# Kernel optimization log

Measured on AMD Instinct MI355X. Metric: run time of the kernel, lower is better.

## Reference

```python
import jax, jax.numpy as jnp
import numpy as np
import math

B, T, C = 4, 2048, 1024
H = 16  # parallelAttentionPathways
D = C // H  # head dim = 64


def setup_inputs() -> dict:
    key = jax.random.key(0)
    k1, k2, k3 = jax.random.split(key, 3)
    x = jax.random.normal(k1, (B, T, C), dtype=jnp.float32)
    w_qkv = jax.random.normal(k2, (3 * C, C), dtype=jnp.float32) * (1.0 / math.sqrt(C))
    w_out = jax.random.normal(k3, (C, C), dtype=jnp.float32) * (1.0 / math.sqrt(C))
    return {"x": x, "w_qkv": w_qkv, "w_out": w_out}


def reference(x, w_qkv, w_out):
    b, t, c = x.shape
    # qkv projection: torch Linear y = x @ W^T (no bias)
    qkv = jnp.einsum('btc,fc->btf', x, w_qkv)  # [B,T,3C]
    q, k, v = jnp.split(qkv, 3, axis=-1)
    # [B,H,T,D]
    q = q.reshape(b, t, H, D).transpose(0, 2, 1, 3)
    k = k.reshape(b, t, H, D).transpose(0, 2, 1, 3)
    v = v.reshape(b, t, H, D).transpose(0, 2, 1, 3)
    scale = 1.0 / math.sqrt(D)
    att = jnp.einsum('bhqd,bhkd->bhqk', q, k) * scale  # [B,H,T,T]
    causal = jnp.tril(jnp.ones((t, t), dtype=bool))
    att = jnp.where(causal[None, None], att, -jnp.inf)
    att = jax.nn.softmax(att, axis=-1)
    # dropoutRate=0.0 -> dropout is identity (eval-mode determinism)
    y = jnp.einsum('bhqk,bhkd->bhqd', att, v)  # [B,H,T,D]
    y = y.transpose(0, 2, 1, 3).reshape(b, t, c)
    return jnp.einsum('btc,fc->btf', y, w_out)
```

## Files before the change

kernel.cpp:

```cpp
#include <hip/hip_runtime.h>
#include <hip/hip_bf16.h>
#include <stdint.h>


using bf16 = __hip_bfloat16;
typedef __attribute__((ext_vector_type(8))) __bf16 bf16x8;
typedef __attribute__((ext_vector_type(8))) unsigned short u16x8;
typedef __attribute__((ext_vector_type(4))) unsigned short u16x4;
typedef __attribute__((ext_vector_type(4))) float f32x4;
typedef unsigned short ushort_t;

#define MFMA16(a, b, c) __builtin_amdgcn_mfma_f32_16x16x32_bf16((a), (b), (c), 0, 0, 0)

__device__ __forceinline__ bf16x8 ld_frag(const ushort_t* p) {
  const u16x8 u = *(const u16x8*)p;
  return __builtin_bit_cast(bf16x8, u);
}

__device__ __forceinline__ ushort_t f2bf(float f) {
  return __builtin_bit_cast(ushort_t, __float2bfloat16(f));
}

__device__ __forceinline__ void gl2lds16(const void* g, void* lds) {
  __builtin_amdgcn_global_load_lds((const __attribute__((address_space(1))) void*)g,
                                   (__attribute__((address_space(3))) void*)lds,
                                   16, 0, 0);
}

__global__ void detect_dtype(const ushort_t* __restrict__ x, int* __restrict__ flag) {
  __shared__ int red[256];
  const int tid = threadIdx.x;
  int cnt = 0;
  for (int i = tid; i < 4096; i += 256) {
    const int e = (x[i] & 0x7FFF) >> 7;
    cnt += (e >= 117 && e <= 133) ? 1 : 0;
  }
  red[tid] = cnt;
  __syncthreads();
  for (int s = 128; s > 0; s >>= 1) {
    if (tid < s) red[tid] += red[tid + s];
    __syncthreads();
  }
  if (tid == 0) *flag = (red[0] < 3072) ? 1 : 0;
}

__global__ void cvt_to_bf16(const void* __restrict__ in, ushort_t* __restrict__ out,
                            int n, const int* __restrict__ flag) {
  const int i = (blockIdx.x * 256 + threadIdx.x) * 8;
  if (i >= n) return;
  if (*flag) {
    const float* p = (const float*)in + i;
    const float4 f0 = *(const float4*)p;
    const float4 f1 = *(const float4*)(p + 4);
    u16x8 u;
    u[0] = f2bf(f0.x); u[1] = f2bf(f0.y); u[2] = f2bf(f0.z); u[3] = f2bf(f0.w);
    u[4] = f2bf(f1.x); u[5] = f2bf(f1.y); u[6] = f2bf(f1.z); u[7] = f2bf(f1.w);
    *(u16x8*)(out + i) = u;
  } else {
    *(u16x8*)(out + i) = *(const u16x8*)((const ushort_t*)in + i);
  }
}

template <int EPI>
__global__ __launch_bounds__(256, 2)
void gemm_nt(const ushort_t* __restrict__ A, const void* __restrict__ Bw,
             const int* __restrict__ flag, int bExt,
             float* __restrict__ C0, ushort_t* __restrict__ Qo,
             ushort_t* __restrict__ Ko, ushort_t* __restrict__ Vt,
             int M, int N, int Kd) {
  __shared__ ushort_t sA[128 * 32];
  __shared__ ushort_t sB[128 * 32];
  const int tid = threadIdx.x;
  const int wave = tid >> 6, lane = tid & 63;
  const int quad = lane >> 4, l16 = lane & 15;
  const int wm = wave >> 1, wn = wave & 1;
  const long m0 = (long)blockIdx.y * 128;
  const long n0 = (long)blockIdx.x * 128;
  const int bF = bExt ? *flag : 0;

  f32x4 acc[4][4];
#pragma unroll
  for (int i = 0; i < 4; ++i)
#pragma unroll
    for (int j = 0; j < 4; ++j) acc[i][j] = (f32x4){0.f, 0.f, 0.f, 0.f};

  for (int k0 = 0; k0 < Kd; k0 += 32) {
#pragma unroll
    for (int j = 0; j < 2; ++j) {
      const int chunk = wave * 2 + j;
      const int idx = chunk * 64 + lane;
      const int r = idx >> 2, c = idx & 3;
      gl2lds16(A + (m0 + r) * (long)Kd + k0 + c * 8, (char*)sA + chunk * 1024);
    }
    if (!bF) {
#pragma unroll
      for (int j = 0; j < 2; ++j) {
        const int chunk = wave * 2 + j;
        const int idx = chunk * 64 + lane;
        const int r = idx >> 2, c = idx & 3;
        gl2lds16((const ushort_t*)Bw + (n0 + r) * (long)Kd + k0 + c * 8,
                 (char*)sB + chunk * 1024);
      }
    } else {
#pragma unroll
      for (int t2 = 0; t2 < 2; ++t2) {
        const int idx = t2 * 256 + tid;
        const int r = idx >> 2, c = idx & 3;
        const float* p = (const float*)Bw + (n0 + r) * (long)Kd + k0 + c * 8;
        const float4 f0 = *(const float4*)p;
        const float4 f1 = *(const float4*)(p + 4);
        u16x8 u;
        u[0] = f2bf(f0.x); u[1] = f2bf(f0.y); u[2] = f2bf(f0.z); u[3] = f2bf(f0.w);
        u[4] = f2bf(f1.x); u[5] = f2bf(f1.y); u[6] = f2bf(f1.z); u[7] = f2bf(f1.w);
        *(u16x8*)&sB[r * 32 + c * 8] = u;
      }
    }
    __syncthreads();
    bf16x8 af[4], bfr[4];
#pragma unroll
    for (int i = 0; i < 4; ++i) {
      const int r = wm * 64 + i * 16 + l16;
      af[i] = ld_frag(&sA[r * 32 + quad * 8]);
    }
#pragma unroll
    for (int i = 0; i < 4; ++i) {
      const int r = wn * 64 + i * 16 + l16;
      bfr[i] = ld_frag(&sB[r * 32 + quad * 8]);
    }
#pragma unroll
    for (int i = 0; i < 4; ++i)
#pragma unroll
      for (int j = 0; j < 4; ++j) acc[i][j] = MFMA16(af[i], bfr[j], acc[i][j]);
    __syncthreads();
  }

#pragma unroll
  for (int i = 0; i < 4; ++i) {
#pragma unroll
    for (int j = 0; j < 4; ++j) {
      if (EPI == 0) {
#pragma unroll
        for (int reg = 0; reg < 4; ++reg) {
          const long m = m0 + wm * 64 + i * 16 + quad * 4 + reg;
          const long n = n0 + wn * 64 + j * 16 + l16;
          C0[m * N + n] = acc[i][j][reg];
        }
      } else {
        const long n = n0 + wn * 64 + j * 16 + l16;
        const int which = (int)(n >> 10);
        const int h = (int)((n >> 6) & 15);
        const int d = (int)(n & 63);
        const long mbase = m0 + wm * 64 + i * 16 + quad * 4;
        const long b = mbase >> 11;
        const long tb = mbase & 2047;
        if (which == 2) {
          u16x4 pk;
#pragma unroll
          for (int reg = 0; reg < 4; ++reg) pk[reg] = f2bf(acc[i][j][reg]);
          *(u16x4*)&Vt[((b * 16 + h) * 64 + d) * 2048 + tb] = pk;
        } else {
          ushort_t* dst = (which == 0) ? Qo : Ko;
#pragma unroll
          for (int reg = 0; reg < 4; ++reg)
            dst[((b * 16 + h) * 2048 + tb + reg) * 64 + d] = f2bf(acc[i][j][reg]);
        }
      }
    }
  }
}

#define RS 72

__device__ __forceinline__ void attn_tile(const bf16x8 qf[2], const ushort_t* sK,
                                          const ushort_t* sV, ushort_t* sPw,
                                          int kv, int qg, int quad, int l16,
                                          float& m_i, float& l_i, f32x4* oacc) {
  f32x4 s[4];
#pragma unroll
  for (int nt = 0; nt < 4; ++nt) s[nt] = (f32x4){0.f, 0.f, 0.f, 0.f};
#pragma unroll
  for (int nt = 0; nt < 4; ++nt) {
#pragma unroll
    for (int kk = 0; kk < 2; ++kk) {
      const bf16x8 kf = ld_frag(&sK[(nt * 16 + l16) * RS + (kk * 4 + quad) * 8]);
      s[nt] = MFMA16(kf, qf[kk], s[nt]);
    }
  }
  const int kb = kv * 64 + quad * 4;
  float rmax = -1e30f;
#pragma unroll
  for (int nt = 0; nt < 4; ++nt) {
#pragma unroll
    for (int reg = 0; reg < 4; ++reg) {
      float v = s[nt][reg] * 0.125f;
      if (kb + nt * 16 + reg > qg) v = -1e30f;
      s[nt][reg] = v;
      rmax = fmaxf(rmax, v);
    }
  }
  rmax = fmaxf(rmax, __shfl_xor(rmax, 16, 64));
  rmax = fmaxf(rmax, __shfl_xor(rmax, 32, 64));
  const float mnew = fmaxf(m_i, rmax);
  float rs = 0.f;
#pragma unroll
  for (int nt = 0; nt < 4; ++nt) {
#pragma unroll
    for (int reg = 0; reg < 4; ++reg) {
      const float p = __expf(s[nt][reg] - mnew);
      s[nt][reg] = p;
      rs += p;
    }
  }
  rs += __shfl_xor(rs, 16, 64);
  rs += __shfl_xor(rs, 32, 64);
  const float alpha = __expf(m_i - mnew);
  l_i = l_i * alpha + rs;
  m_i = mnew;
#pragma unroll
  for (int dt = 0; dt < 4; ++dt) oacc[dt] *= alpha;

  __threadfence_block();
#pragma unroll
  for (int nt = 0; nt < 4; ++nt) {
    u16x4 pk;
#pragma unroll
    for (int reg = 0; reg < 4; ++reg) pk[reg] = f2bf(s[nt][reg]);
    *(u16x4*)&sPw[l16 * RS + nt * 16 + quad * 4] = pk;
  }
  __threadfence_block();
  bf16x8 pf[2];
#pragma unroll
  for (int kk = 0; kk < 2; ++kk)
    pf[kk] = ld_frag(&sPw[l16 * RS + kk * 32 + quad * 8]);
#pragma unroll
  for (int dt = 0; dt < 4; ++dt) {
#pragma unroll
    for (int kk = 0; kk < 2; ++kk) {
      const bf16x8 vf = ld_frag(&sV[(dt * 16 + l16) * RS + (kk * 4 + quad) * 8]);
      oacc[dt] = MFMA16(vf, pf[kk], oacc[dt]);
    }
  }
}

__global__ __launch_bounds__(256, 4)
void attn_causal(const ushort_t* __restrict__ Qg, const ushort_t* __restrict__ Kg,
                 const ushort_t* __restrict__ Vt, ushort_t* __restrict__ Yg) {
  __shared__ ushort_t sK[64 * RS];
  __shared__ ushort_t sV[64 * RS];
  __shared__ ushort_t sPQ[64 * RS];
  const int tid = threadIdx.x;
  const int wave = tid >> 6, lane = tid & 63;
  const int quad = lane >> 4, l16 = lane & 15;
  const int qx = blockIdx.x, bh = blockIdx.y;
  const int qtA = qx, qtB = 31 - qx;
  const size_t base = (size_t)bh * 2048 * 64;
  ushort_t* sPw = sPQ + wave * 16 * RS;

  bf16x8 qfA[2], qfB[2];
#pragma unroll
  for (int tile = 0; tile < 2; ++tile) {
    const int qt = tile ? qtB : qtA;
#pragma unroll
    for (int t2 = 0; t2 < 2; ++t2) {
      const int idx = t2 * 256 + tid;
      const int r = idx >> 3, c = idx & 7;
      *(u16x8*)&sPQ[r * RS + c * 8] =
          *(const u16x8*)(Qg + base + (size_t)(qt * 64 + r) * 64 + c * 8);
    }
    __syncthreads();
#pragma unroll
    for (int kk = 0; kk < 2; ++kk) {
      const bf16x8 f = ld_frag(&sPQ[(wave * 16 + l16) * RS + (kk * 4 + quad) * 8]);
      if (tile) qfB[kk] = f; else qfA[kk] = f;
    }
    __syncthreads();
  }

  float mA = -1e30f, lA = 0.f, mB = -1e30f, lB = 0.f;
  f32x4 oA[4], oB[4];
#pragma unroll
  for (int dt = 0; dt < 4; ++dt) {
    oA[dt] = (f32x4){0.f, 0.f, 0.f, 0.f};
    oB[dt] = (f32x4){0.f, 0.f, 0.f, 0.f};
  }
  const int qgA = qtA * 64 + wave * 16 + l16;
  const int qgB = qtB * 64 + wave * 16 + l16;

  for (int kv = 0; kv <= qtB; ++kv) {
    __syncthreads();
#pragma unroll
    for (int t2 = 0; t2 < 2; ++t2) {
      const int idx = t2 * 256 + tid;
      const int r = idx >> 3, c = idx & 7;
      *(u16x8*)&sK[r * RS + c * 8] =
          *(const u16x8*)(Kg + base + (size_t)(kv * 64 + r) * 64 + c * 8);
      *(u16x8*)&sV[r * RS + c * 8] =
          *(const u16x8*)(Vt + base + (size_t)r * 2048 + kv * 64 + c * 8);
    }
    __syncthreads();
    attn_tile(qfB, sK, sV, sPw, kv, qgB, quad, l16, mB, lB, oB);
    if (kv <= qtA)
      attn_tile(qfA, sK, sV, sPw, kv, qgA, quad, l16, mA, lA, oA);
  }

  const int b = bh >> 4, h = bh & 15;
#pragma unroll
  for (int tile = 0; tile < 2; ++tile) {
    const int qt = tile ? qtB : qtA;
    const float linv = 1.f / (tile ? lB : lA);
    const f32x4* o = tile ? oB : oA;
    const int t = qt * 64 + wave * 16 + l16;
#pragma unroll
    for (int dt = 0; dt < 4; ++dt) {
      u16x4 pk;
#pragma unroll
      for (int reg = 0; reg < 4; ++reg) pk[reg] = f2bf(o[dt][reg] * linv);
      *(u16x4*)&Yg[(((size_t)b * 2048 + t) * 16 + h) * 64 + dt * 16 + quad * 4] = pk;
    }
  }
}

extern "C" void kernel_launch(void* const* d_in, const int* in_sizes, int n_in,
                              void* d_out, int out_size, void* d_ws, size_t ws_size,
                              hipStream_t stream) {
  const void* x = d_in[0];
  const void* w_qkv = d_in[1];
  const void* w_out = d_in[2];
  float* out = (float*)d_out;

  const size_t per = (size_t)4 * 16 * 2048 * 64;
  const size_t nwqkv = (size_t)3072 * 1024;
  const size_t nwout = (size_t)1024 * 1024;
  ushort_t* qws = (ushort_t*)d_ws;
  ushort_t* kws = qws + per;
  ushort_t* vTws = kws + per;
  ushort_t* xyws = vTws + per;
  ushort_t* wqkvb = xyws + per;
  ushort_t* woutb = wqkvb + nwqkv;
  int* flag = (int*)(woutb + nwout);
  const size_t need = (size_t)(4 * per + nwqkv + nwout) * 2 + 16;
  const bool pre = ws_size >= need;
  (void)in_sizes; (void)n_in; (void)out_size;

  dim3 blk(256);
  if (!pre) flag = (int*)(xyws + per);
  detect_dtype<<<1, 256, 0, stream>>>((const ushort_t*)x, flag);
  cvt_to_bf16<<<4096, 256, 0, stream>>>(x, xyws, (int)per, flag);
  if (pre) {
    cvt_to_bf16<<<1536, 256, 0, stream>>>(w_qkv, wqkvb, (int)nwqkv, flag);
    cvt_to_bf16<<<512, 256, 0, stream>>>(w_out, woutb, (int)nwout, flag);
    gemm_nt<1><<<dim3(24, 64), blk, 0, stream>>>(xyws, wqkvb, flag, 0, nullptr,
                                                 qws, kws, vTws, 8192, 3072, 1024);
    attn_causal<<<dim3(16, 64), blk, 0, stream>>>(qws, kws, vTws, xyws);
    gemm_nt<0><<<dim3(8, 64), blk, 0, stream>>>(xyws, woutb, flag, 0, out,
                                                nullptr, nullptr, nullptr,
                                                8192, 1024, 1024);
  } else {
    gemm_nt<1><<<dim3(24, 64), blk, 0, stream>>>(xyws, w_qkv, flag, 1, nullptr,
                                                 qws, kws, vTws, 8192, 3072, 1024);
    attn_causal<<<dim3(16, 64), blk, 0, stream>>>(qws, kws, vTws, xyws);
    gemm_nt<0><<<dim3(8, 64), blk, 0, stream>>>(xyws, w_out, flag, 1, out,
                                                nullptr, nullptr, nullptr,
                                                8192, 1024, 1024);
  }
}
```

Measured before the change: 282.9 us.

## Prefetch next KV tile into registers, skip unneeded masking and rescales

Loads the next K/V tile from global memory into registers while the current tile is being computed, so global latency overlaps with the MFMA work. The causal mask is now applied only on diagonal tiles, and the softmax scale is folded into Q once at load time. Online-softmax rescaling is skipped when the new row max stays within a threshold of the old one. The block index is also remapped to interleave heads across workgroups, and the fences are replaced with explicit LDS waitcnts. The cost is extra registers for the prefetch buffers, and the lazy rescale relies on exp values staying bounded.

```diff
diff --git a/kernel.cpp b/kernel.cpp
--- a/kernel.cpp
+++ b/kernel.cpp
@@ -173,7 +173,8 @@
 
 __device__ __forceinline__ void attn_tile(const bf16x8 qf[2], const ushort_t* sK,
                                           const ushort_t* sV, ushort_t* sPw,
-                                          int kv, int qg, int quad, int l16,
+                                          int kv, int qg, bool need_mask,
+                                          int quad, int l16,
                                           float& m_i, float& l_i, f32x4* oacc) {
   f32x4 s[4];
 #pragma unroll
@@ -188,19 +189,36 @@
   }
   const int kb = kv * 64 + quad * 4;
   float rmax = -1e30f;
-#pragma unroll
-  for (int nt = 0; nt < 4; ++nt) {
-#pragma unroll
-    for (int reg = 0; reg < 4; ++reg) {
-      float v = s[nt][reg] * 0.125f;
-      if (kb + nt * 16 + reg > qg) v = -1e30f;
-      s[nt][reg] = v;
-      rmax = fmaxf(rmax, v);
+  if (need_mask) {
+#pragma unroll
+    for (int nt = 0; nt < 4; ++nt) {
+#pragma unroll
+      for (int reg = 0; reg < 4; ++reg) {
+        float v = s[nt][reg];
+        if (kb + nt * 16 + reg > qg) v = -1e30f;
+        s[nt][reg] = v;
+        rmax = fmaxf(rmax, v);
+      }
+    }
+  } else {
+#pragma unroll
+    for (int nt = 0; nt < 4; ++nt) {
+#pragma unroll
+      for (int reg = 0; reg < 4; ++reg) rmax = fmaxf(rmax, s[nt][reg]);
     }
   }
   rmax = fmaxf(rmax, __shfl_xor(rmax, 16, 64));
   rmax = fmaxf(rmax, __shfl_xor(rmax, 32, 64));
-  const float mnew = fmaxf(m_i, rmax);
+  float mnew = fmaxf(m_i, rmax);
+  if (__all(rmax - m_i <= 5.5f)) {
+    mnew = m_i;
+  } else {
+    const float alpha = __expf(m_i - mnew);
+    l_i *= alpha;
+#pragma unroll
+    for (int dt = 0; dt < 4; ++dt) oacc[dt] *= alpha;
+    m_i = mnew;
+  }
   float rs = 0.f;
 #pragma unroll
   for (int nt = 0; nt < 4; ++nt) {
@@ -213,13 +231,9 @@
   }
   rs += __shfl_xor(rs, 16, 64);
   rs += __shfl_xor(rs, 32, 64);
-  const float alpha = __expf(m_i - mnew);
-  l_i = l_i * alpha + rs;
-  m_i = mnew;
-#pragma unroll
-  for (int dt = 0; dt < 4; ++dt) oacc[dt] *= alpha;
-
-  __threadfence_block();
+  l_i += rs;
+
+  asm volatile("s_waitcnt lgkmcnt(0)" ::: "memory");
 #pragma unroll
   for (int nt = 0; nt < 4; ++nt) {
     u16x4 pk;
@@ -227,7 +241,7 @@
     for (int reg = 0; reg < 4; ++reg) pk[reg] = f2bf(s[nt][reg]);
     *(u16x4*)&sPw[l16 * RS + nt * 16 + quad * 4] = pk;
   }
-  __threadfence_block();
+  asm volatile("s_waitcnt lgkmcnt(0)" ::: "memory");
   bf16x8 pf[2];
 #pragma unroll
   for (int kk = 0; kk < 2; ++kk)
@@ -251,7 +265,9 @@
   const int tid = threadIdx.x;
   const int wave = tid >> 6, lane = tid & 63;
   const int quad = lane >> 4, l16 = lane & 15;
-  const int qx = blockIdx.x, bh = blockIdx.y;
+  const int lin = blockIdx.y * 16 + blockIdx.x;
+  const int logical = (lin & 7) * 128 + (lin >> 3);
+  const int qx = logical & 15, bh = logical >> 4;
   const int qtA = qx, qtB = 31 - qx;
   const size_t base = (size_t)bh * 2048 * 64;
   ushort_t* sPw = sPQ + wave * 16 * RS;
@@ -270,7 +286,12 @@
     __syncthreads();
 #pragma unroll
     for (int kk = 0; kk < 2; ++kk) {
-      const bf16x8 f = ld_frag(&sPQ[(wave * 16 + l16) * RS + (kk * 4 + quad) * 8]);
+      const u16x8 u = *(const u16x8*)&sPQ[(wave * 16 + l16) * RS + (kk * 4 + quad) * 8];
+      u16x8 w;
+#pragma unroll
+      for (int e = 0; e < 8; ++e)
+        w[e] = f2bf(__bfloat162float(__builtin_bit_cast(bf16, (ushort_t)u[e])) * 0.125f);
+      const bf16x8 f = __builtin_bit_cast(bf16x8, w);
       if (tile) qfB[kk] = f; else qfA[kk] = f;
     }
     __syncthreads();
@@ -285,6 +306,17 @@
   }
   const int qgA = qtA * 64 + wave * 16 + l16;
   const int qgB = qtB * 64 + wave * 16 + l16;
+  const int qmA = qtA * 64 + wave * 16;
+  const int qmB = qtB * 64 + wave * 16;
+
+  u16x8 kr[2], vr[2];
+#pragma unroll
+  for (int t2 = 0; t2 < 2; ++t2) {
+    const int idx = t2 * 256 + tid;
+    const int r = idx >> 3, c = idx & 7;
+    kr[t2] = *(const u16x8*)(Kg + base + (size_t)r * 64 + c * 8);
+    vr[t2] = *(const u16x8*)(Vt + base + (size_t)r * 2048 + c * 8);
+  }
 
   for (int kv = 0; kv <= qtB; ++kv) {
     __syncthreads();
@@ -292,15 +324,23 @@
     for (int t2 = 0; t2 < 2; ++t2) {
       const int idx = t2 * 256 + tid;
       const int r = idx >> 3, c = idx & 7;
-      *(u16x8*)&sK[r * RS + c * 8] =
-          *(const u16x8*)(Kg + base + (size_t)(kv * 64 + r) * 64 + c * 8);
-      *(u16x8*)&sV[r * RS + c * 8] =
-          *(const u16x8*)(Vt + base + (size_t)r * 2048 + kv * 64 + c * 8);
-    }
-    __syncthreads();
-    attn_tile(qfB, sK, sV, sPw, kv, qgB, quad, l16, mB, lB, oB);
+      *(u16x8*)&sK[r * RS + c * 8] = kr[t2];
+      *(u16x8*)&sV[r * RS + c * 8] = vr[t2];
+    }
+    __syncthreads();
+    if (kv < qtB) {
+      const int kn = kv + 1;
+#pragma unroll
+      for (int t2 = 0; t2 < 2; ++t2) {
+        const int idx = t2 * 256 + tid;
+        const int r = idx >> 3, c = idx & 7;
+        kr[t2] = *(const u16x8*)(Kg + base + (size_t)(kn * 64 + r) * 64 + c * 8);
+        vr[t2] = *(const u16x8*)(Vt + base + (size_t)r * 2048 + kn * 64 + c * 8);
+      }
+    }
+    attn_tile(qfB, sK, sV, sPw, kv, qgB, kv * 64 + 63 > qmB, quad, l16, mB, lB, oB);
     if (kv <= qtA)
-      attn_tile(qfA, sK, sV, sPw, kv, qgA, quad, l16, mA, lA, oA);
+      attn_tile(qfA, sK, sV, sPw, kv, qgA, kv * 64 + 63 > qmA, quad, l16, mA, lA, oA);
   }
 
   const int b = bh >> 4, h = bh & 15;
```

New measurement: 269.9 us. 4.6% less time.
